# Optimization experiments

Measured on AMD Instinct MI355X. Metric: run time of the kernel, lower is better.

The kernel has to match this reference:

```python
import jax, jax.numpy as jnp
import numpy as np

SIGMA = 1.0          # args.sigma
THRESH = 0.35        # hard-coded stop threshold in gat_selection_feature
MAX_ITERS = 48       # bound on the data-dependent greedy loop (gain saturates to 0)


def setup_inputs() -> dict:
    key = jax.random.key(0)
    k1, k2, k3, k4 = jax.random.split(key, 4)
    B, N, F = 8192, 64, 32  # dst nodes, neighbors per node, feature size (attn_weights is 32x1)
    return {
        "mail": jax.random.normal(k1, (B, N, F), jnp.float32),
        "attn_w": jax.random.normal(k2, (F, 1), jnp.float32),
        "src_norm": jax.random.uniform(k3, (B, N), jnp.float32, minval=0.5, maxval=1.0),
        "dst_norm": jax.random.uniform(k4, (B,), jnp.float32, minval=0.5, maxval=1.0),
    }


def _pairwise_dist(x):
    # torch.cdist: Euclidean pairwise distances, [B,N,F] -> [B,N,N]
    sq = jnp.sum(x * x, axis=-1)
    d2 = sq[:, :, None] + sq[:, None, :] - 2.0 * jnp.einsum('bnf,bmf->bnm', x, x)
    return jnp.sqrt(jnp.maximum(d2, 0.0))


def reference(mail, attn_w, src_norm, dst_norm):
    # source-degree normalization (degs^-0.5 applied to feat_src before update_all)
    feat = mail * src_norm[..., None]                     # [B,N,F]
    B, N, Fd = feat.shape

    dists = _pairwise_dist(feat)                          # [B,N,N]
    mean_d = dists.mean(axis=(-2, -1))[:, None, None]     # per-batch scalar mean
    sims = jnp.exp(-dists / (SIGMA * mean_d))             # [B,N,N]

    # attention_weights(features): constant across greedy iterations
    logits = jnp.einsum('bnf,fo->bn', feat, attn_w)       # [B,N]
    attention = jax.nn.softmax(logits, axis=1)            # [B,N]

    bidx = jnp.arange(B)

    def step(carry, _):
        cache, acc, active = carry                        # cache [B,N], acc [B,F], active scalar bool
        gain = jnp.sum(jnp.maximum(sims, cache[:, None, :]) - cache[:, None, :], axis=-1)
        gain = gain * attention                           # [B,N]
        max_value = gain.max()
        sel = jnp.argmax(gain, axis=1)                    # [B]
        w = jnp.where(active, jnp.float32(1.0), jnp.float32(0.0))
        acc = acc + w * feat[bidx, sel]                   # append-then-check: terminating iter included
        cache = jnp.where(active, jnp.maximum(sims[bidx, sel], cache), cache)
        active = jnp.logical_and(active, max_value >= THRESH)
        return (cache, acc, active), None

    cache0 = jnp.zeros((B, N), feat.dtype)
    acc0 = jnp.zeros((B, Fd), feat.dtype)
    (_, acc, _), _ = jax.lax.scan(step, (cache0, acc0, jnp.array(True)), None, length=MAX_ITERS)

    # destination in-degree normalization
    return acc * dst_norm[:, None]
```

## Files before the change

### kernel.cpp

```cpp
#include <hip/hip_runtime.h>

#define B_TOT 8192
#define NN 64
#define FF 32
#define ITERS 48
#define THRESH 0.35f

#define TSTOP_OFF (458752)
#define ATTN_OFF  (524288)
#define SIMS_OFF  (4194304)
#define WS_NEEDED (SIMS_OFF + (size_t)B_TOT * NN * NN * 4)

__global__ __launch_bounds__(64) void gat_greedy_kernel(
    const float* __restrict__ mail,
    const float* __restrict__ attn_w,
    const float* __restrict__ src_norm,
    int* __restrict__ tmax_ws,
    unsigned char* __restrict__ sels_ws)
{
    const int b = blockIdx.x;
    const int lane = threadIdx.x;

    __shared__ __align__(16) float sims[NN * 65];
    __shared__ __align__(16) float c_lds[NN];
    __shared__ float qarr[NN];
    __shared__ float sarr[NN];

    const float* __restrict__ myrow = mail + ((size_t)b * NN + lane) * FF;
    float a[FF];
#pragma unroll
    for (int k = 0; k < 8; ++k) {
        const float4 v = reinterpret_cast<const float4*>(myrow)[k];
        a[4*k+0] = v.x; a[4*k+1] = v.y; a[4*k+2] = v.z; a[4*k+3] = v.w;
    }
    const float sn = src_norm[b * NN + lane];

    float q0 = 0.f, q1 = 0.f, q2 = 0.f, q3 = 0.f;
#pragma unroll
    for (int k = 0; k < 8; ++k) {
        q0 = fmaf(a[4*k+0], a[4*k+0], q0);
        q1 = fmaf(a[4*k+1], a[4*k+1], q1);
        q2 = fmaf(a[4*k+2], a[4*k+2], q2);
        q3 = fmaf(a[4*k+3], a[4*k+3], q3);
    }
    const float q = (q0 + q1) + (q2 + q3);

    float lg = 0.f;
#pragma unroll
    for (int f = 0; f < FF; ++f) lg = fmaf(a[f], attn_w[f], lg);
    lg *= sn;

    qarr[lane] = q;
    sarr[lane] = sn;
    __syncthreads();

    float mx = lg;
#pragma unroll
    for (int off = 32; off > 0; off >>= 1)
        mx = fmaxf(mx, __shfl_xor(mx, off, 64));
    const float ex = __expf(lg - mx);
    float se = ex;
#pragma unroll
    for (int off = 32; off > 0; off >>= 1)
        se += __shfl_xor(se, off, 64);
    const float attn = ex / se;

    const float sqn = sn * sn * q;
    float dsum = 0.f;
    for (int m = 0; m < NN; ++m) {
        const float4* __restrict__ Am =
            reinterpret_cast<const float4*>(mail + ((size_t)b * NN + m) * FF);
        float g0 = 0.f, g1 = 0.f, g2 = 0.f, g3 = 0.f;
#pragma unroll
        for (int k = 0; k < 8; ++k) {
            const float4 v = Am[k];
            g0 = fmaf(a[4*k+0], v.x, g0);
            g1 = fmaf(a[4*k+1], v.y, g1);
            g2 = fmaf(a[4*k+2], v.z, g2);
            g3 = fmaf(a[4*k+3], v.w, g3);
        }
        const float g  = (g0 + g1) + (g2 + g3);
        const float sm = sarr[m];
        const float qm = qarr[m];
        const float sqm = sm * sm * qm;
        const float d2  = (sqn - 2.f * (sn * sm) * g) + sqm;
        const float d   = sqrtf(fmaxf(d2, 0.f));
        dsum += d;
        sims[lane * 65 + m] = d;
    }

    float tot = dsum;
#pragma unroll
    for (int off = 32; off > 0; off >>= 1)
        tot += __shfl_xor(tot, off, 64);
    const float meand = tot * (1.f / (float)(NN * NN));
    const float inv   = -1.f / meand;

    float srow[NN];
#pragma unroll
    for (int m = 0; m < NN; ++m) {
        const float d = sims[lane * 65 + m];
        const float s = __expf(d * inv);
        srow[m] = s;
        sims[lane * 65 + m] = s;
    }
#pragma unroll
    for (int m = 0; m < NN; ++m)
        asm volatile("" : "+v"(srow[m]));

    c_lds[lane] = 0.f;
    float c_reg = 0.f;
    __syncthreads();

    int firstBelow = ITERS;
    bool seenBelow = false;

    for (int t = 0; t < ITERS; ++t) {
        float gain = 0.f;
#pragma unroll
        for (int k = 0; k < 16; ++k) {
            const float4 cv = reinterpret_cast<const float4*>(c_lds)[k];
            gain += fmaxf(srow[4*k+0] - cv.x, 0.f);
            gain += fmaxf(srow[4*k+1] - cv.y, 0.f);
            gain += fmaxf(srow[4*k+2] - cv.z, 0.f);
            gain += fmaxf(srow[4*k+3] - cv.w, 0.f);
        }
        gain *= attn;

        float gv = gain; int gi = lane;
#pragma unroll
        for (int off = 32; off > 0; off >>= 1) {
            const float ov = __shfl_xor(gv, off, 64);
            const int   oi = __shfl_xor(gi, off, 64);
            if (ov > gv || (ov == gv && oi < gi)) { gv = ov; gi = oi; }
        }

        if (!seenBelow && gv < THRESH) { firstBelow = t; seenBelow = true; }
        if (lane == 0) sels_ws[(size_t)b * ITERS + t] = (unsigned char)gi;

        const float srl = sims[gi * 65 + lane];
        c_reg = fmaxf(c_reg, srl);
        c_lds[lane] = c_reg;
        __syncthreads();
    }

    if (lane == 0) atomicMax(tmax_ws, firstBelow);
}

__global__ __launch_bounds__(64) void gat_fusedA_kernel(
    const float* __restrict__ mail,
    const float* __restrict__ attn_w,
    const float* __restrict__ src_norm,
    int* __restrict__ tmax_ws,
    int* __restrict__ tstop_ws,
    unsigned char* __restrict__ sels_ws,
    float* __restrict__ sims_g,
    float* __restrict__ attn_g)
{
    const int b = blockIdx.x;
    const int lane = threadIdx.x;

    __shared__ __align__(16) float sims[NN * 65];
    __shared__ __align__(16) float c_lds[NN];
    __shared__ float qarr[NN];
    __shared__ float sarr[NN];

    const float* __restrict__ myrow = mail + ((size_t)b * NN + lane) * FF;
    float a[FF];
#pragma unroll
    for (int k = 0; k < 8; ++k) {
        const float4 v = reinterpret_cast<const float4*>(myrow)[k];
        a[4*k+0] = v.x; a[4*k+1] = v.y; a[4*k+2] = v.z; a[4*k+3] = v.w;
    }
    const float sn = src_norm[b * NN + lane];

    float q0 = 0.f, q1 = 0.f, q2 = 0.f, q3 = 0.f;
#pragma unroll
    for (int k = 0; k < 8; ++k) {
        q0 = fmaf(a[4*k+0], a[4*k+0], q0);
        q1 = fmaf(a[4*k+1], a[4*k+1], q1);
        q2 = fmaf(a[4*k+2], a[4*k+2], q2);
        q3 = fmaf(a[4*k+3], a[4*k+3], q3);
    }
    const float q = (q0 + q1) + (q2 + q3);

    float lg = 0.f;
#pragma unroll
    for (int f = 0; f < FF; ++f) lg = fmaf(a[f], attn_w[f], lg);
    lg *= sn;

    qarr[lane] = q;
    sarr[lane] = sn;
    __syncthreads();

    float mx = lg;
#pragma unroll
    for (int off = 32; off > 0; off >>= 1)
        mx = fmaxf(mx, __shfl_xor(mx, off, 64));
    const float ex = __expf(lg - mx);
    float se = ex;
#pragma unroll
    for (int off = 32; off > 0; off >>= 1)
        se += __shfl_xor(se, off, 64);
    const float attn = ex / se;

    attn_g[b * NN + lane] = attn;

    const float sqn = sn * sn * q;
    float dsum = 0.f;
    for (int m = 0; m < NN; ++m) {
        const float4* __restrict__ Am =
            reinterpret_cast<const float4*>(mail + ((size_t)b * NN + m) * FF);
        float g0 = 0.f, g1 = 0.f, g2 = 0.f, g3 = 0.f;
#pragma unroll
        for (int k = 0; k < 8; ++k) {
            const float4 v = Am[k];
            g0 = fmaf(a[4*k+0], v.x, g0);
            g1 = fmaf(a[4*k+1], v.y, g1);
            g2 = fmaf(a[4*k+2], v.z, g2);
            g3 = fmaf(a[4*k+3], v.w, g3);
        }
        const float g  = (g0 + g1) + (g2 + g3);
        const float sm = sarr[m];
        const float qm = qarr[m];
        const float sqm = sm * sm * qm;
        const float d2  = (sqn - 2.f * (sn * sm) * g) + sqm;
        const float d   = sqrtf(fmaxf(d2, 0.f));
        dsum += d;
        sims[lane * 65 + m] = d;
    }

    float tot = dsum;
#pragma unroll
    for (int off = 32; off > 0; off >>= 1)
        tot += __shfl_xor(tot, off, 64);
    const float meand = tot * (1.f / (float)(NN * NN));
    const float inv   = -1.f / meand;

    float* __restrict__ Tb = sims_g + (size_t)b * NN * NN;
    float srow[NN];
#pragma unroll
    for (int m = 0; m < NN; ++m) {
        const float d = sims[lane * 65 + m];
        const float s = __expf(d * inv);
        srow[m] = s;
        sims[lane * 65 + m] = s;
        Tb[m * NN + lane] = s;
    }
#pragma unroll
    for (int m = 0; m < NN; ++m)
        asm volatile("" : "+v"(srow[m]));

    c_lds[lane] = 0.f;
    float c_reg = 0.f;
    __syncthreads();

    int firstBelow = ITERS;

    for (int t = 0; t < ITERS; ++t) {
        float gain = 0.f;
#pragma unroll
        for (int k = 0; k < 16; ++k) {
            const float4 cv = reinterpret_cast<const float4*>(c_lds)[k];
            gain += fmaxf(srow[4*k+0] - cv.x, 0.f);
            gain += fmaxf(srow[4*k+1] - cv.y, 0.f);
            gain += fmaxf(srow[4*k+2] - cv.z, 0.f);
            gain += fmaxf(srow[4*k+3] - cv.w, 0.f);
        }
        gain *= attn;

        float gv = gain; int gi = lane;
#pragma unroll
        for (int off = 32; off > 0; off >>= 1) {
            const float ov = __shfl_xor(gv, off, 64);
            const int   oi = __shfl_xor(gi, off, 64);
            if (ov > gv || (ov == gv && oi < gi)) { gv = ov; gi = oi; }
        }

        if (lane == 0) sels_ws[(size_t)b * ITERS + t] = (unsigned char)gi;

        const float srl = sims[gi * 65 + lane];
        c_reg = fmaxf(c_reg, srl);
        c_lds[lane] = c_reg;
        __syncthreads();

        if (gv < THRESH) { firstBelow = t; break; }
    }

    if (lane == 0) {
        atomicMax(tmax_ws, firstBelow);
        tstop_ws[b] = firstBelow;
    }
}

__global__ __launch_bounds__(64) void gat_greedyB_acc_kernel(
    const float* __restrict__ sims_g,
    const float* __restrict__ attn_g,
    const float* __restrict__ mail,
    const float* __restrict__ src_norm,
    const float* __restrict__ dst_norm,
    const int* __restrict__ tmax_ws,
    const int* __restrict__ tstop_ws,
    const unsigned char* __restrict__ sels_ws,
    float* __restrict__ out)
{
    const int b = blockIdx.x;
    const int lane = threadIdx.x;

    const int fb   = tstop_ws[b];
    const int Tmax = *tmax_ws;
    const int tEnd = min(ITERS - 1, Tmax);

    __shared__ __align__(16) float sims[NN * 65];
    __shared__ __align__(16) float c_lds[NN];
    __shared__ int sel_lds[ITERS];

    const unsigned char* __restrict__ sb = sels_ws + (size_t)b * ITERS;

    if (fb < tEnd) {
        const float* __restrict__ Tb = sims_g + (size_t)b * NN * NN;

        float srow[NN];
#pragma unroll
        for (int c = 0; c < NN; ++c) {
            const float v = Tb[c * NN + lane];
            sims[lane * 65 + c] = v;
            srow[c] = v;
        }
#pragma unroll
        for (int m = 0; m < NN; ++m)
            asm volatile("" : "+v"(srow[m]));

        const float attn = attn_g[b * NN + lane];

        float c_reg = 0.f;
        __syncthreads();
        for (int j = 0; j <= fb; ++j) {
            const int sel = sb[j];
            c_reg = fmaxf(c_reg, sims[sel * 65 + lane]);
        }
        c_lds[lane] = c_reg;
        __syncthreads();

        for (int t = fb + 1; t <= tEnd; ++t) {
            float gain = 0.f;
#pragma unroll
            for (int k = 0; k < 16; ++k) {
                const float4 cv = reinterpret_cast<const float4*>(c_lds)[k];
                gain += fmaxf(srow[4*k+0] - cv.x, 0.f);
                gain += fmaxf(srow[4*k+1] - cv.y, 0.f);
                gain += fmaxf(srow[4*k+2] - cv.z, 0.f);
                gain += fmaxf(srow[4*k+3] - cv.w, 0.f);
            }
            gain *= attn;

            float gv = gain; int gi = lane;
#pragma unroll
            for (int off = 32; off > 0; off >>= 1) {
                const float ov = __shfl_xor(gv, off, 64);
                const int   oi = __shfl_xor(gi, off, 64);
                if (ov > gv || (ov == gv && oi < gi)) { gv = ov; gi = oi; }
            }

            if (lane == 0) sel_lds[t] = gi;

            const float srl = sims[gi * 65 + lane];
            c_reg = fmaxf(c_reg, srl);
            c_lds[lane] = c_reg;
            __syncthreads();
        }
    }

    if (lane < FF) {
        const int C = min(ITERS, Tmax + 1);
        float acc = 0.f;
        for (int t = 0; t < C; ++t) {
            const int sel = (t <= fb) ? (int)sb[t] : sel_lds[t];
            acc = fmaf(mail[((size_t)b * NN + sel) * FF + lane],
                       src_norm[b * NN + sel], acc);
        }
        out[b * FF + lane] = acc * dst_norm[b];
    }
}

__global__ __launch_bounds__(64) void gat_accum_kernel(
    const float* __restrict__ mail,
    const float* __restrict__ src_norm,
    const float* __restrict__ dst_norm,
    const int* __restrict__ tmax_ws,
    const unsigned char* __restrict__ sels_ws,
    float* __restrict__ out)
{
    const int lane = threadIdx.x & 31;
    const int b = blockIdx.x * 2 + (threadIdx.x >> 5);
    const int C = min(ITERS, *tmax_ws + 1);
    const unsigned char* __restrict__ sb = sels_ws + (size_t)b * ITERS;
    float acc = 0.f;
    for (int t = 0; t < C; ++t) {
        const int sel = sb[t];
        acc = fmaf(mail[((size_t)b * NN + sel) * FF + lane],
                   src_norm[b * NN + sel], acc);
    }
    out[b * FF + lane] = acc * dst_norm[b];
}

extern "C" void kernel_launch(void* const* d_in, const int* in_sizes, int n_in,
                              void* d_out, int out_size, void* d_ws, size_t ws_size,
                              hipStream_t stream)
{
    const float* mail     = (const float*)d_in[0];
    const float* attn_w   = (const float*)d_in[1];
    const float* src_norm = (const float*)d_in[2];
    const float* dst_norm = (const float*)d_in[3];
    float* out = (float*)d_out;

    int* tmax_ws = (int*)d_ws;
    unsigned char* sels_ws = (unsigned char*)d_ws + 16;

    hipMemsetAsync(d_ws, 0, 4, stream);

    if (ws_size >= WS_NEEDED) {
        int*   tstop_ws = (int*)((char*)d_ws + TSTOP_OFF);
        float* attn_g   = (float*)((char*)d_ws + ATTN_OFF);
        float* sims_g   = (float*)((char*)d_ws + SIMS_OFF);
        gat_fusedA_kernel<<<dim3(B_TOT), dim3(64), 0, stream>>>(
            mail, attn_w, src_norm, tmax_ws, tstop_ws, sels_ws, sims_g, attn_g);
        gat_greedyB_acc_kernel<<<dim3(B_TOT), dim3(64), 0, stream>>>(
            sims_g, attn_g, mail, src_norm, dst_norm,
            tmax_ws, tstop_ws, sels_ws, out);
    } else {
        gat_greedy_kernel<<<dim3(B_TOT), dim3(64), 0, stream>>>(
            mail, attn_w, src_norm, tmax_ws, sels_ws);
        gat_accum_kernel<<<dim3(B_TOT / 2), dim3(64), 0, stream>>>(
            mail, src_norm, dst_norm, tmax_ws, sels_ws, out);
    }
}
```

Measured before the change: 240.7 us.

## Drop LDS sims tile; store distance matrix globally and recompute exp on demand

Removes the 16.6KB shared-memory similarity tile from both fused kernels. Kernel A now writes raw distances to global memory, rereads them to build register rows, and stores the per-batch inverse mean. Selected-row lookups recompute exp from global (L2-cached) distances instead of reading LDS. The aim is higher occupancy from lower LDS use, at the cost of extra global round trips and exp work on the serial greedy critical path.

```diff
diff --git a/kernel.cpp b/kernel.cpp
--- a/kernel.cpp
+++ b/kernel.cpp
@@ -7,6 +7,7 @@
 #define THRESH 0.35f
 
 #define TSTOP_OFF (458752)
+#define INV_OFF   (491520)
 #define ATTN_OFF  (524288)
 #define SIMS_OFF  (4194304)
 #define WS_NEEDED (SIMS_OFF + (size_t)B_TOT * NN * NN * 4)
@@ -154,13 +155,13 @@
     int* __restrict__ tmax_ws,
     int* __restrict__ tstop_ws,
     unsigned char* __restrict__ sels_ws,
-    float* __restrict__ sims_g,
-    float* __restrict__ attn_g)
+    float* __restrict__ dmat_g,
+    float* __restrict__ attn_g,
+    float* __restrict__ inv_g)
 {
     const int b = blockIdx.x;
     const int lane = threadIdx.x;
 
-    __shared__ __align__(16) float sims[NN * 65];
     __shared__ __align__(16) float c_lds[NN];
     __shared__ float qarr[NN];
     __shared__ float sarr[NN];
@@ -205,6 +206,8 @@
     const float attn = ex / se;
 
     attn_g[b * NN + lane] = attn;
+
+    float* __restrict__ Tb = dmat_g + (size_t)b * NN * NN;
 
     const float sqn = sn * sn * q;
     float dsum = 0.f;
@@ -227,7 +230,7 @@
         const float d2  = (sqn - 2.f * (sn * sm) * g) + sqm;
         const float d   = sqrtf(fmaxf(d2, 0.f));
         dsum += d;
-        sims[lane * 65 + m] = d;
+        Tb[m * NN + lane] = d;
     }
 
     float tot = dsum;
@@ -237,15 +240,14 @@
     const float meand = tot * (1.f / (float)(NN * NN));
     const float inv   = -1.f / meand;
 
-    float* __restrict__ Tb = sims_g + (size_t)b * NN * NN;
+    if (lane == 0) inv_g[b] = inv;
+
     float srow[NN];
 #pragma unroll
     for (int m = 0; m < NN; ++m) {
-        const float d = sims[lane * 65 + m];
+        const float d = Tb[m * NN + lane];
         const float s = __expf(d * inv);
         srow[m] = s;
-        sims[lane * 65 + m] = s;
-        Tb[m * NN + lane] = s;
     }
 #pragma unroll
     for (int m = 0; m < NN; ++m)
@@ -279,7 +281,7 @@
 
         if (lane == 0) sels_ws[(size_t)b * ITERS + t] = (unsigned char)gi;
 
-        const float srl = sims[gi * 65 + lane];
+        const float srl = __expf(Tb[lane * NN + gi] * inv);
         c_reg = fmaxf(c_reg, srl);
         c_lds[lane] = c_reg;
         __syncthreads();
@@ -294,8 +296,9 @@
 }
 
 __global__ __launch_bounds__(64) void gat_greedyB_acc_kernel(
-    const float* __restrict__ sims_g,
+    const float* __restrict__ dmat_g,
     const float* __restrict__ attn_g,
+    const float* __restrict__ inv_g,
     const float* __restrict__ mail,
     const float* __restrict__ src_norm,
     const float* __restrict__ dst_norm,
@@ -311,22 +314,19 @@
     const int Tmax = *tmax_ws;
     const int tEnd = min(ITERS - 1, Tmax);
 
-    __shared__ __align__(16) float sims[NN * 65];
     __shared__ __align__(16) float c_lds[NN];
     __shared__ int sel_lds[ITERS];
 
     const unsigned char* __restrict__ sb = sels_ws + (size_t)b * ITERS;
 
     if (fb < tEnd) {
-        const float* __restrict__ Tb = sims_g + (size_t)b * NN * NN;
+        const float* __restrict__ Tb = dmat_g + (size_t)b * NN * NN;
+        const float inv = inv_g[b];
 
         float srow[NN];
 #pragma unroll
-        for (int c = 0; c < NN; ++c) {
-            const float v = Tb[c * NN + lane];
-            sims[lane * 65 + c] = v;
-            srow[c] = v;
-        }
+        for (int c = 0; c < NN; ++c)
+            srow[c] = __expf(Tb[c * NN + lane] * inv);
 #pragma unroll
         for (int m = 0; m < NN; ++m)
             asm volatile("" : "+v"(srow[m]));
@@ -334,10 +334,9 @@
         const float attn = attn_g[b * NN + lane];
 
         float c_reg = 0.f;
-        __syncthreads();
         for (int j = 0; j <= fb; ++j) {
             const int sel = sb[j];
-            c_reg = fmaxf(c_reg, sims[sel * 65 + lane]);
+            c_reg = fmaxf(c_reg, __expf(Tb[lane * NN + sel] * inv));
         }
         c_lds[lane] = c_reg;
         __syncthreads();
@@ -364,7 +363,7 @@
 
             if (lane == 0) sel_lds[t] = gi;
 
-            const float srl = sims[gi * 65 + lane];
+            const float srl = __expf(Tb[lane * NN + gi] * inv);
             c_reg = fmaxf(c_reg, srl);
             c_lds[lane] = c_reg;
             __syncthreads();
@@ -421,12 +420,14 @@
 
     if (ws_size >= WS_NEEDED) {
         int*   tstop_ws = (int*)((char*)d_ws + TSTOP_OFF);
+        float* inv_g    = (float*)((char*)d_ws + INV_OFF);
         float* attn_g   = (float*)((char*)d_ws + ATTN_OFF);
-        float* sims_g   = (float*)((char*)d_ws + SIMS_OFF);
+        float* dmat_g   = (float*)((char*)d_ws + SIMS_OFF);
         gat_fusedA_kernel<<<dim3(B_TOT), dim3(64), 0, stream>>>(
-            mail, attn_w, src_norm, tmax_ws, tstop_ws, sels_ws, sims_g, attn_g);
+            mail, attn_w, src_norm, tmax_ws, tstop_ws, sels_ws,
+            dmat_g, attn_g, inv_g);
         gat_greedyB_acc_kernel<<<dim3(B_TOT), dim3(64), 0, stream>>>(
-            sims_g, attn_g, mail, src_norm, dst_norm,
+            dmat_g, attn_g, inv_g, mail, src_norm, dst_norm,
             tmax_ws, tstop_ws, sels_ws, out);
     } else {
         gat_greedy_kernel<<<dim3(B_TOT), dim3(64), 0, stream>>>(
```

After: 270.7 us. 12.5% more time.
